# Optimization experiments

Hardware: AMD Instinct MI355X
Metric: run time of the kernel (lower is better)

## Reference

```python
import jax, jax.numpy as jnp
import numpy as np

B, S, D, F, E, K = 2, 1024, 2048, 8192, 4, 2  # batch, seq, d_model, d_ff, n_experts, top_k


def setup_inputs() -> dict:
    key = jax.random.key(0)
    k0, k1, k2, k3, k4 = jax.random.split(key, 5)
    scaled = lambda k, shape, fan_in: (jax.random.normal(k, shape, jnp.float32) * (fan_in ** -0.5))
    return {
        "x": jax.random.normal(k0, (B, S, D), jnp.float32),
        "Wr": scaled(k1, (D, E), D),          # router (gating_layer.gate) weight
        "Wg": scaled(k2, (E, D, F), D),        # stacked expert gate_proj weights
        "Wu": scaled(k3, (E, D, F), D),        # stacked expert up_proj weights
        "Wd": scaled(k4, (E, F, D), F),        # stacked expert down_proj weights
    }


def reference(x, Wr, Wg, Wu, Wd):
    # Router: softmax over expert logits, take top-k values + indices
    probs = jax.nn.softmax(x @ Wr, axis=-1)                 # [B,S,E]
    gate_vals, gate_idx = jax.lax.top_k(probs, K)           # [B,S,K] each

    # Dense per-expert SwiGLU MLP for EVERY token (faithful to the original loop)
    g = jax.nn.silu(jnp.einsum('bsd,edf->bsef', x, Wg))     # [B,S,E,F]
    u = jnp.einsum('bsd,edf->bsef', x, Wu)                  # [B,S,E,F]
    eo = jnp.einsum('bsef,efd->bsed', g * u, Wd)            # [B,S,E,D]

    # Gather the top-k experts per token, scale by gate values, sum (combine)
    idx = jnp.broadcast_to(gate_idx[..., None], (B, S, K, D))
    sel = jnp.take_along_axis(eo, idx, axis=2)              # [B,S,K,D]
    return (sel * gate_vals[..., None]).sum(axis=2)         # [B,S,D]
```

## Files before the change

kernel.cpp:

```cpp
#include <hip/hip_runtime.h>
#include <stdint.h>


#define T_TOK 2048
#define DM    2048
#define FF    8192

typedef unsigned short u16;
typedef short short8 __attribute__((ext_vector_type(8)));
typedef float f32x4  __attribute__((ext_vector_type(4)));

#define GLL16(g, l) __builtin_amdgcn_global_load_lds( \
    (const __attribute__((address_space(1))) void*)(g), \
    (__attribute__((address_space(3))) void*)(l), 16, 0, 0)

__device__ __forceinline__ u16 f2bf(float f) {
  uint32_t x = __float_as_uint(f);
  x += 0x7fffu + ((x >> 16) & 1u);
  return (u16)(x >> 16);
}

__global__ __launch_bounds__(256) void router_kernel(
    const float* __restrict__ x, const float* __restrict__ Wr,
    int* __restrict__ counts, int* __restrict__ tok, float* __restrict__ gate)
{
  int t = blockIdx.x * 4 + (threadIdx.x >> 6);
  int l = threadIdx.x & 63;
  const float* xr = x + (size_t)t * DM;
  const float4* wr4 = (const float4*)Wr;
  float a0 = 0.f, a1 = 0.f, a2 = 0.f, a3 = 0.f;
  for (int d = l; d < DM; d += 64) {
    float xv = xr[d];
    float4 w = wr4[d];
    a0 += xv * w.x; a1 += xv * w.y; a2 += xv * w.z; a3 += xv * w.w;
  }
  #pragma unroll
  for (int off = 32; off > 0; off >>= 1) {
    a0 += __shfl_down(a0, off);
    a1 += __shfl_down(a1, off);
    a2 += __shfl_down(a2, off);
    a3 += __shfl_down(a3, off);
  }
  if (l == 0) {
    float lg[4] = {a0, a1, a2, a3};
    float m = fmaxf(fmaxf(lg[0], lg[1]), fmaxf(lg[2], lg[3]));
    float p[4], s = 0.f;
    #pragma unroll
    for (int e = 0; e < 4; ++e) { p[e] = __expf(lg[e] - m); s += p[e]; }
    #pragma unroll
    for (int e = 0; e < 4; ++e) p[e] /= s;
    int i0 = 0;
    #pragma unroll
    for (int e = 1; e < 4; ++e) if (p[e] > p[i0]) i0 = e;
    int i1 = (i0 == 0) ? 1 : 0;
    #pragma unroll
    for (int e = 0; e < 4; ++e) if (e != i0 && p[e] > p[i1]) i1 = e;
    int s0 = atomicAdd(&counts[i0], 1);
    tok[i0 * T_TOK + s0] = t; gate[i0 * T_TOK + s0] = p[i0];
    int s1 = atomicAdd(&counts[i1], 1);
    tok[i1 * T_TOK + s1] = t; gate[i1 * T_TOK + s1] = p[i1];
  }
}

__global__ __launch_bounds__(256) void gather_kernel(
    const float* __restrict__ x, const int* __restrict__ counts,
    const int* __restrict__ tok, u16* __restrict__ Xe)
{
  int e = blockIdx.x >> 11;
  int slot = blockIdx.x & (T_TOK - 1);
  if (slot >= counts[e]) return;
  int t = tok[e * T_TOK + slot];
  const float4* src = (const float4*)(x + (size_t)t * DM);
  u16* dst = Xe + ((size_t)e * T_TOK + slot) * DM;
  int i = threadIdx.x;
  float4 a = src[i * 2], b = src[i * 2 + 1];
  union { u16 h[8]; uint4 q; } v;
  v.h[0] = f2bf(a.x); v.h[1] = f2bf(a.y); v.h[2] = f2bf(a.z); v.h[3] = f2bf(a.w);
  v.h[4] = f2bf(b.x); v.h[5] = f2bf(b.y); v.h[6] = f2bf(b.z); v.h[7] = f2bf(b.w);
  *(uint4*)(dst + i * 8) = v.q;
}

__global__ __launch_bounds__(256) void trans_cvt_kernel(
    const float* __restrict__ src, u16* __restrict__ dst, int R, int C)
{
  __shared__ float tile[64][65];
  int c0 = blockIdx.x * 64, r0 = blockIdx.y * 64;
  int tid = threadIdx.x;
  int tc = tid & 63, tr = tid >> 6;
  #pragma unroll
  for (int i = 0; i < 16; ++i) {
    int row = i * 4 + tr;
    tile[row][tc] = src[(size_t)(r0 + row) * C + c0 + tc];
  }
  __syncthreads();
  int wr = tid & 15, rr = tid >> 4;
  #pragma unroll
  for (int i = 0; i < 4; ++i) {
    int row = i * 16 + rr;
    ushort4 v;
    v.x = f2bf(tile[wr * 4 + 0][row]);
    v.y = f2bf(tile[wr * 4 + 1][row]);
    v.z = f2bf(tile[wr * 4 + 2][row]);
    v.w = f2bf(tile[wr * 4 + 3][row]);
    *(ushort4*)&dst[(size_t)(c0 + row) * R + r0 + wr * 4] = v;
  }
}

__global__ __launch_bounds__(256, 2) void gemm12_kernel(
    const u16* __restrict__ A, const u16* __restrict__ Bg, const u16* __restrict__ Bu,
    u16* __restrict__ H, const int* __restrict__ cntp)
{
  const int cnt = *cntp;
  if ((int)blockIdx.y * 128 >= cnt) return;
  __shared__ __align__(16) u16 As[128 * 64];
  __shared__ __align__(16) u16 Bgs[128 * 64];
  __shared__ __align__(16) u16 Bus[128 * 64];
  const int tid = threadIdx.x, l = tid & 63, w = tid >> 6;
  const int wm = w & 1, wn = w >> 1;
  const int cg = (l & 7) ^ (l >> 3);
  const u16* ap[4]; const u16* bgp[4]; const u16* bup[4];
  const u16* la[4]; const u16* lbg[4]; const u16* lbu[4];
  #pragma unroll
  for (int j = 0; j < 4; ++j) {
    int r0 = (w * 4 + j) * 8;
    int row = r0 + (l >> 3);
    ap[j]  = A  + (size_t)(blockIdx.y * 128 + row) * DM + cg * 8;
    bgp[j] = Bg + (size_t)(blockIdx.x * 128 + row) * DM + cg * 8;
    bup[j] = Bu + (size_t)(blockIdx.x * 128 + row) * DM + cg * 8;
    la[j]  = As  + r0 * 64;
    lbg[j] = Bgs + r0 * 64;
    lbu[j] = Bus + r0 * 64;
  }
  int fm[4], fn[4];
  #pragma unroll
  for (int i = 0; i < 4; ++i) {
    fm[i] = (wm * 64 + i * 16 + (l & 15)) * 64;
    fn[i] = (wn * 64 + i * 16 + (l & 15)) * 64;
  }
  f32x4 accg[4][4] = {};
  f32x4 accu[4][4] = {};
  for (int kt = 0; kt < DM / 64; ++kt) {
    #pragma unroll
    for (int j = 0; j < 4; ++j) {
      GLL16(ap[j]  + kt * 64, la[j]);
      GLL16(bgp[j] + kt * 64, lbg[j]);
      GLL16(bup[j] + kt * 64, lbu[j]);
    }
    __syncthreads();
    #pragma unroll
    for (int kk = 0; kk < 2; ++kk) {
      const int c2 = ((kk * 4 + (l >> 4)) ^ (l & 7)) * 8;
      short8 af[4], bgf[4], buf_[4];
      #pragma unroll
      for (int i = 0; i < 4; ++i) af[i]   = *(const short8*)&As[fm[i] + c2];
      #pragma unroll
      for (int i = 0; i < 4; ++i) bgf[i]  = *(const short8*)&Bgs[fn[i] + c2];
      #pragma unroll
      for (int i = 0; i < 4; ++i) buf_[i] = *(const short8*)&Bus[fn[i] + c2];
      #pragma unroll
      for (int mt = 0; mt < 4; ++mt)
        #pragma unroll
        for (int nt = 0; nt < 4; ++nt) {
          accg[mt][nt] = __builtin_amdgcn_mfma_f32_16x16x32_bf16(af[mt], bgf[nt],  accg[mt][nt], 0, 0, 0);
          accu[mt][nt] = __builtin_amdgcn_mfma_f32_16x16x32_bf16(af[mt], buf_[nt], accu[mt][nt], 0, 0, 0);
        }
    }
    __syncthreads();
  }
  const int rbase = blockIdx.y * 128 + wm * 64 + ((l >> 4) << 2);
  const int cbase = blockIdx.x * 128 + wn * 64 + (l & 15);
  #pragma unroll
  for (int mt = 0; mt < 4; ++mt) {
    #pragma unroll
    for (int i = 0; i < 4; ++i) {
      int r = rbase + mt * 16 + i;
      u16* hrow = H + (size_t)r * FF + cbase;
      #pragma unroll
      for (int nt = 0; nt < 4; ++nt) {
        float g = accg[mt][nt][i], u = accu[mt][nt][i];
        float h = (g / (1.f + __expf(-g))) * u;
        hrow[nt * 16] = f2bf(h);
      }
    }
  }
}

__global__ __launch_bounds__(256, 2) void gemm3_kernel(
    const u16* __restrict__ A, const u16* __restrict__ B,
    float* __restrict__ out, const int* __restrict__ cntp,
    const int* __restrict__ tokd, const float* __restrict__ gated)
{
  const int cnt = *cntp;
  if ((int)blockIdx.y * 128 >= cnt) return;
  __shared__ __align__(16) u16 As[128 * 64];
  __shared__ __align__(16) u16 Bs[128 * 64];
  const int tid = threadIdx.x, l = tid & 63, w = tid >> 6;
  const int wm = w & 1, wn = w >> 1;
  const int cg = (l & 7) ^ (l >> 3);
  const u16* ap[4]; const u16* bp[4]; const u16* la[4]; const u16* lb[4];
  #pragma unroll
  for (int j = 0; j < 4; ++j) {
    int r0 = (w * 4 + j) * 8;
    int row = r0 + (l >> 3);
    ap[j] = A + (size_t)(blockIdx.y * 128 + row) * FF + cg * 8;
    bp[j] = B + (size_t)(blockIdx.x * 128 + row) * FF + cg * 8;
    la[j] = As + r0 * 64;
    lb[j] = Bs + r0 * 64;
  }
  int fm[4], fn[4];
  #pragma unroll
  for (int i = 0; i < 4; ++i) {
    fm[i] = (wm * 64 + i * 16 + (l & 15)) * 64;
    fn[i] = (wn * 64 + i * 16 + (l & 15)) * 64;
  }
  f32x4 acc[4][4] = {};
  for (int kt = 0; kt < FF / 64; ++kt) {
    #pragma unroll
    for (int j = 0; j < 4; ++j) {
      GLL16(ap[j] + kt * 64, la[j]);
      GLL16(bp[j] + kt * 64, lb[j]);
    }
    __syncthreads();
    #pragma unroll
    for (int kk = 0; kk < 2; ++kk) {
      const int c2 = ((kk * 4 + (l >> 4)) ^ (l & 7)) * 8;
      short8 af[4], bf[4];
      #pragma unroll
      for (int i = 0; i < 4; ++i) af[i] = *(const short8*)&As[fm[i] + c2];
      #pragma unroll
      for (int i = 0; i < 4; ++i) bf[i] = *(const short8*)&Bs[fn[i] + c2];
      #pragma unroll
      for (int mt = 0; mt < 4; ++mt)
        #pragma unroll
        for (int nt = 0; nt < 4; ++nt)
          acc[mt][nt] = __builtin_amdgcn_mfma_f32_16x16x32_bf16(af[mt], bf[nt], acc[mt][nt], 0, 0, 0);
    }
    __syncthreads();
  }
  const int rbase = blockIdx.y * 128 + wm * 64 + ((l >> 4) << 2);
  const int cbase = blockIdx.x * 128 + wn * 64 + (l & 15);
  #pragma unroll
  for (int mt = 0; mt < 4; ++mt) {
    #pragma unroll
    for (int i = 0; i < 4; ++i) {
      int r = rbase + mt * 16 + i;
      if (r < cnt) {
        int t = tokd[r];
        float gv = gated[r];
        float* orow = out + (size_t)t * DM + cbase;
        #pragma unroll
        for (int nt = 0; nt < 4; ++nt)
          atomicAdd(orow + nt * 16, acc[mt][nt][i] * gv);
      }
    }
  }
}

extern "C" void kernel_launch(void* const* d_in, const int* in_sizes, int n_in,
                              void* d_out, int out_size, void* d_ws, size_t ws_size,
                              hipStream_t stream) {
  (void)in_sizes; (void)n_in; (void)out_size; (void)ws_size;
  const float* x  = (const float*)d_in[0];
  const float* Wr = (const float*)d_in[1];
  const float* Wg = (const float*)d_in[2];
  const float* Wu = (const float*)d_in[3];
  const float* Wd = (const float*)d_in[4];
  float* out = (float*)d_out;

  char* ws = (char*)d_ws;
  int*   counts = (int*)(ws);
  int*   tok    = (int*)(ws + 1024);
  float* gate   = (float*)(ws + 1024 + 4 * T_TOK * 4);
  u16*   Xe     = (u16*)(ws + 1024 + 2 * 4 * T_TOK * 4);
  u16*   Wgt    = Xe  + (size_t)4 * T_TOK * DM;
  u16*   Wut    = Wgt + (size_t)FF * DM;
  u16*   Wdt    = Wut + (size_t)FF * DM;
  u16*   H      = Wdt + (size_t)DM * FF;
  const size_t DF = (size_t)DM * FF;

  hipMemsetAsync(out, 0, (size_t)T_TOK * DM * sizeof(float), stream);
  hipMemsetAsync(counts, 0, 4 * sizeof(int), stream);

  router_kernel<<<T_TOK / 4, 256, 0, stream>>>(x, Wr, counts, tok, gate);
  gather_kernel<<<4 * T_TOK, 256, 0, stream>>>(x, counts, tok, Xe);

  for (int e = 0; e < 4; ++e) {
    trans_cvt_kernel<<<dim3(FF / 64, DM / 64), 256, 0, stream>>>(Wg + e * DF, Wgt, DM, FF);
    trans_cvt_kernel<<<dim3(FF / 64, DM / 64), 256, 0, stream>>>(Wu + e * DF, Wut, DM, FF);
    trans_cvt_kernel<<<dim3(DM / 64, FF / 64), 256, 0, stream>>>(Wd + e * DF, Wdt, FF, DM);
    gemm12_kernel<<<dim3(FF / 128, T_TOK / 128), 256, 0, stream>>>(
        Xe + (size_t)e * T_TOK * DM, Wgt, Wut, H, counts + e);
    gemm3_kernel<<<dim3(DM / 128, T_TOK / 128), 256, 0, stream>>>(
        H, Wdt, out, counts + e, tok + e * T_TOK, gate + e * T_TOK);
  }
}
```

Before: 1.665 ms.

## Batch all experts into single transpose, gate-up and down GEMM launches with split-K

Replaces the per-expert loop of fifteen launches with one transpose/convert kernel covering all twelve weight matrices, one gate/up GEMM indexed by expert in grid y, and one down GEMM that also splits the K dimension in two via grid z. This removes launch serialization and the under-filled grids that appear when an expert has few tokens, letting experts run concurrently on the GPU. In exchange the workspace must hold all experts' converted weights and H buffers at once, and split-K doubles the atomic adds into the output.

```diff
diff --git a/kernel.cpp b/kernel.cpp
--- a/kernel.cpp
+++ b/kernel.cpp
@@ -5,6 +5,7 @@
 #define T_TOK 2048
 #define DM    2048
 #define FF    8192
+#define DF    ((size_t)DM * FF)
 
 typedef unsigned short u16;
 typedef short short8 __attribute__((ext_vector_type(8)));
@@ -80,11 +81,20 @@
   *(uint4*)(dst + i * 8) = v.q;
 }
 
-__global__ __launch_bounds__(256) void trans_cvt_kernel(
-    const float* __restrict__ src, u16* __restrict__ dst, int R, int C)
-{
+__global__ __launch_bounds__(256) void trans_cvt_all(
+    const float* __restrict__ Wg, const float* __restrict__ Wu, const float* __restrict__ Wd,
+    u16* __restrict__ Wgt, u16* __restrict__ Wut, u16* __restrict__ Wdt)
+{
+  int j = blockIdx.y;
+  const float* src; u16* dst; int R, C, clog;
+  if (j < 4)      { src = Wg + (size_t)j * DF;       dst = Wgt + (size_t)j * DF;       R = DM; C = FF; clog = 7; }
+  else if (j < 8) { src = Wu + (size_t)(j - 4) * DF; dst = Wut + (size_t)(j - 4) * DF; R = DM; C = FF; clog = 7; }
+  else            { src = Wd + (size_t)(j - 8) * DF; dst = Wdt + (size_t)(j - 8) * DF; R = FF; C = DM; clog = 5; }
+  int bx = blockIdx.x;
+  int c0 = (bx & ((1 << clog) - 1)) * 64;
+  int r0 = (bx >> clog) * 64;
+
   __shared__ float tile[64][65];
-  int c0 = blockIdx.x * 64, r0 = blockIdx.y * 64;
   int tid = threadIdx.x;
   int tc = tid & 63, tr = tid >> 6;
   #pragma unroll
@@ -107,11 +117,18 @@
 }
 
 __global__ __launch_bounds__(256, 2) void gemm12_kernel(
-    const u16* __restrict__ A, const u16* __restrict__ Bg, const u16* __restrict__ Bu,
-    u16* __restrict__ H, const int* __restrict__ cntp)
-{
-  const int cnt = *cntp;
-  if ((int)blockIdx.y * 128 >= cnt) return;
+    const u16* __restrict__ XeB, const u16* __restrict__ WgtB, const u16* __restrict__ WutB,
+    u16* __restrict__ HB, const int* __restrict__ counts)
+{
+  const int e  = blockIdx.y >> 4;
+  const int rb = blockIdx.y & 15;
+  const int cnt = counts[e];
+  if (rb * 128 >= cnt) return;
+  const u16* A  = XeB + (size_t)e * T_TOK * DM;
+  const u16* Bg = WgtB + (size_t)e * DF;
+  const u16* Bu = WutB + (size_t)e * DF;
+  u16* H = HB + (size_t)e * T_TOK * FF;
+
   __shared__ __align__(16) u16 As[128 * 64];
   __shared__ __align__(16) u16 Bgs[128 * 64];
   __shared__ __align__(16) u16 Bus[128 * 64];
@@ -124,7 +141,7 @@
   for (int j = 0; j < 4; ++j) {
     int r0 = (w * 4 + j) * 8;
     int row = r0 + (l >> 3);
-    ap[j]  = A  + (size_t)(blockIdx.y * 128 + row) * DM + cg * 8;
+    ap[j]  = A  + (size_t)(rb * 128 + row) * DM + cg * 8;
     bgp[j] = Bg + (size_t)(blockIdx.x * 128 + row) * DM + cg * 8;
     bup[j] = Bu + (size_t)(blockIdx.x * 128 + row) * DM + cg * 8;
     la[j]  = As  + r0 * 64;
@@ -167,7 +184,7 @@
     }
     __syncthreads();
   }
-  const int rbase = blockIdx.y * 128 + wm * 64 + ((l >> 4) << 2);
+  const int rbase = rb * 128 + wm * 64 + ((l >> 4) << 2);
   const int cbase = blockIdx.x * 128 + wn * 64 + (l & 15);
   #pragma unroll
   for (int mt = 0; mt < 4; ++mt) {
@@ -186,12 +203,20 @@
 }
 
 __global__ __launch_bounds__(256, 2) void gemm3_kernel(
-    const u16* __restrict__ A, const u16* __restrict__ B,
-    float* __restrict__ out, const int* __restrict__ cntp,
-    const int* __restrict__ tokd, const float* __restrict__ gated)
-{
-  const int cnt = *cntp;
-  if ((int)blockIdx.y * 128 >= cnt) return;
+    const u16* __restrict__ HB, const u16* __restrict__ WdtB,
+    float* __restrict__ out, const int* __restrict__ counts,
+    const int* __restrict__ tokB, const float* __restrict__ gateB)
+{
+  const int e  = blockIdx.y >> 4;
+  const int rb = blockIdx.y & 15;
+  const int cnt = counts[e];
+  if (rb * 128 >= cnt) return;
+  const u16* A = HB + (size_t)e * T_TOK * FF;
+  const u16* B = WdtB + (size_t)e * DF;
+  const int* tokd = tokB + e * T_TOK;
+  const float* gated = gateB + e * T_TOK;
+  const int kt0 = blockIdx.z * 64, kt1 = kt0 + 64;
+
   __shared__ __align__(16) u16 As[128 * 64];
   __shared__ __align__(16) u16 Bs[128 * 64];
   const int tid = threadIdx.x, l = tid & 63, w = tid >> 6;
@@ -202,7 +227,7 @@
   for (int j = 0; j < 4; ++j) {
     int r0 = (w * 4 + j) * 8;
     int row = r0 + (l >> 3);
-    ap[j] = A + (size_t)(blockIdx.y * 128 + row) * FF + cg * 8;
+    ap[j] = A + (size_t)(rb * 128 + row) * FF + cg * 8;
     bp[j] = B + (size_t)(blockIdx.x * 128 + row) * FF + cg * 8;
     la[j] = As + r0 * 64;
     lb[j] = Bs + r0 * 64;
@@ -214,7 +239,7 @@
     fn[i] = (wn * 64 + i * 16 + (l & 15)) * 64;
   }
   f32x4 acc[4][4] = {};
-  for (int kt = 0; kt < FF / 64; ++kt) {
+  for (int kt = kt0; kt < kt1; ++kt) {
     #pragma unroll
     for (int j = 0; j < 4; ++j) {
       GLL16(ap[j] + kt * 64, la[j]);
@@ -237,7 +262,7 @@
     }
     __syncthreads();
   }
-  const int rbase = blockIdx.y * 128 + wm * 64 + ((l >> 4) << 2);
+  const int rbase = rb * 128 + wm * 64 + ((l >> 4) << 2);
   const int cbase = blockIdx.x * 128 + wn * 64 + (l & 15);
   #pragma unroll
   for (int mt = 0; mt < 4; ++mt) {
@@ -273,24 +298,16 @@
   float* gate   = (float*)(ws + 1024 + 4 * T_TOK * 4);
   u16*   Xe     = (u16*)(ws + 1024 + 2 * 4 * T_TOK * 4);
   u16*   Wgt    = Xe  + (size_t)4 * T_TOK * DM;
-  u16*   Wut    = Wgt + (size_t)FF * DM;
-  u16*   Wdt    = Wut + (size_t)FF * DM;
-  u16*   H      = Wdt + (size_t)DM * FF;
-  const size_t DF = (size_t)DM * FF;
+  u16*   Wut    = Wgt + 4 * DF;
+  u16*   Wdt    = Wut + 4 * DF;
+  u16*   H      = Wdt + 4 * DF;
 
   hipMemsetAsync(out, 0, (size_t)T_TOK * DM * sizeof(float), stream);
   hipMemsetAsync(counts, 0, 4 * sizeof(int), stream);
 
   router_kernel<<<T_TOK / 4, 256, 0, stream>>>(x, Wr, counts, tok, gate);
   gather_kernel<<<4 * T_TOK, 256, 0, stream>>>(x, counts, tok, Xe);
-
-  for (int e = 0; e < 4; ++e) {
-    trans_cvt_kernel<<<dim3(FF / 64, DM / 64), 256, 0, stream>>>(Wg + e * DF, Wgt, DM, FF);
-    trans_cvt_kernel<<<dim3(FF / 64, DM / 64), 256, 0, stream>>>(Wu + e * DF, Wut, DM, FF);
-    trans_cvt_kernel<<<dim3(DM / 64, FF / 64), 256, 0, stream>>>(Wd + e * DF, Wdt, FF, DM);
-    gemm12_kernel<<<dim3(FF / 128, T_TOK / 128), 256, 0, stream>>>(
-        Xe + (size_t)e * T_TOK * DM, Wgt, Wut, H, counts + e);
-    gemm3_kernel<<<dim3(DM / 128, T_TOK / 128), 256, 0, stream>>>(
-        H, Wdt, out, counts + e, tok + e * T_TOK, gate + e * T_TOK);
-  }
-}
+  trans_cvt_all<<<dim3(4096, 12), 256, 0, stream>>>(Wg, Wu, Wd, Wgt, Wut, Wdt);
+  gemm12_kernel<<<dim3(FF / 128, 64), 256, 0, stream>>>(Xe, Wgt, Wut, H, counts);
+  gemm3_kernel<<<dim3(DM / 128, 64, 2), 256, 0, stream>>>(H, Wdt, out, counts, tok, gate);
+}
```

New measurement: 1.334 ms. 1.25x faster.
